# Optimization experiments

Measured on AMD Instinct MI355X. Metric: run time of the kernel, lower is better.

The kernel has to match this reference:

```python
import jax, jax.numpy as jnp
import numpy as np

B, E, H, KVH, S = 1, 4096, 32, 8, 2048
HD = E // H            # per-head dim = 128
KVE = KVH * HD         # kv projection embed dim = 1024


def setup_inputs() -> dict:
    key = jax.random.key(0)
    ks = jax.random.split(key, 10)
    std = 0.02
    return {
        "input_embeds": jax.random.normal(ks[0], (B, E, 1, S), jnp.float32),
        "cos": jax.random.uniform(ks[1], (HD, S), jnp.float32, -1.0, 1.0),
        "sin": jax.random.uniform(ks[2], (HD, S), jnp.float32, -1.0, 1.0),
        "wq": jax.random.normal(ks[3], (E, E), jnp.float32) * std,
        "bq": jnp.zeros((E,), jnp.float32),
        "wk": jax.random.normal(ks[4], (KVE, E), jnp.float32) * std,
        "wv": jax.random.normal(ks[5], (KVE, E), jnp.float32) * std,
        "bv": jnp.zeros((KVE,), jnp.float32),
        "wo": jax.random.normal(ks[6], (E, E), jnp.float32) * std,
        "bo": jnp.zeros((E,), jnp.float32),
    }


def _proj(w, x, b=None):
    # 1x1 Conv2d == channelwise linear on (B, C, 1, S)
    y = jnp.einsum('oc,bcxs->boxs', w, x)
    if b is not None:
        y = y + b[None, :, None, None]
    return y


def _rope(x, cos, sin):
    # x: (B, h, HD, S); rotate-half along head_dim axis
    half = x.shape[2] // 2
    x1, x2 = x[:, :, :half], x[:, :, half:]
    rot = jnp.concatenate([-x2, x1], axis=2)
    return x * cos[None, None] + rot * sin[None, None]


def reference(input_embeds, cos, sin, wq, bq, wk, wv, bv, wo, bo):
    b, e, _, s = input_embeds.shape
    hd = e // H
    q = _proj(wq, input_embeds, bq)          # (B, E, 1, S)
    k = _proj(wk, input_embeds)              # (B, KVE, 1, S)  (no bias)
    v = _proj(wv, input_embeds, bv)          # (B, KVE, 1, S)

    qh = q.reshape(b, H, hd, s)
    kh = k.reshape(b, KVH, hd, s)
    qh = _rope(qh, cos, sin)
    kh = _rope(kh, cos, sin)

    # GQA tiling: channel-block repeat => query head h uses kv head (h % KVH)
    rep = H // KVH
    kfull = jnp.tile(kh, (1, rep, 1, 1))                       # (B, H, HD, S)
    vfull = jnp.tile(v.reshape(b, KVH, hd, s), (1, rep, 1, 1))  # (B, H, HD, S)

    scale = 1.0 / np.sqrt(hd).astype(np.float32)
    scores = jnp.einsum('bhcq,bhck->bhqk', qh, kfull) * scale  # (B, H, S, S)
    causal = jnp.tril(jnp.ones((s, s), bool))
    scores = jnp.where(causal[None, None], scores, jnp.finfo(scores.dtype).min)
    w = jax.nn.softmax(scores, axis=-1)
    attn = jnp.einsum('bhqk,bhck->bhcq', w, vfull).reshape(b, e, 1, s)
    return _proj(wo, attn, bo)
```

## Files before the change

kernel.cpp:

```cpp
#include <hip/hip_runtime.h>


typedef unsigned short u16;
typedef unsigned int u32;
typedef __attribute__((ext_vector_type(8))) short bf16x8;
typedef __attribute__((ext_vector_type(4))) float f32x4;

__device__ __forceinline__ u16 f2b(float f){
  union { float f; u32 u; } v; v.f = f;
  u32 r = (v.u + 0x7FFFu + ((v.u >> 16) & 1u)) >> 16;
  return (u16)r;
}
__device__ __forceinline__ float b2f(u16 b){
  union { u32 u; float f; } v; v.u = ((u32)b) << 16;
  return v.f;
}

__device__ __forceinline__ void gld16(const void* g, void* l){
  __builtin_amdgcn_global_load_lds((const __attribute__((address_space(1))) u32*)g,
                                   (__attribute__((address_space(3))) u32*)l, 16, 0, 0);
}

__global__ __launch_bounds__(256) void cvt_w(const float* __restrict__ src,
                                             u16* __restrict__ dst, int n4)
{
  int i = blockIdx.x * 256 + threadIdx.x;
  if (i < n4){
    float4 v = *(const float4*)&src[(size_t)i * 4];
    ushort4 o; o.x = f2b(v.x); o.y = f2b(v.y); o.z = f2b(v.z); o.w = f2b(v.w);
    *(ushort4*)&dst[(size_t)i * 4] = o;
  }
}

__global__ __launch_bounds__(256) void transpose_x(const float* __restrict__ X,
                                                   u16* __restrict__ XT)
{
  __shared__ float lds[64][65];
  const int c0 = blockIdx.x * 64, s0 = blockIdx.y * 64;
  const int tid = threadIdx.x;
  {
    const int sg = tid & 15, cl = tid >> 4;
#pragma unroll
    for (int p = 0; p < 4; ++p){
      int c = cl + p * 16;
      float4 v = *(const float4*)&X[(size_t)(c0 + c) * 2048 + s0 + sg * 4];
      lds[sg*4+0][c] = v.x; lds[sg*4+1][c] = v.y;
      lds[sg*4+2][c] = v.z; lds[sg*4+3][c] = v.w;
    }
  }
  __syncthreads();
  {
    const int cg = tid & 15, sl = tid >> 4;
#pragma unroll
    for (int p = 0; p < 4; ++p){
      int s = sl + p * 16;
      ushort4 o;
      o.x = f2b(lds[s][cg*4+0]); o.y = f2b(lds[s][cg*4+1]);
      o.z = f2b(lds[s][cg*4+2]); o.w = f2b(lds[s][cg*4+3]);
      *(ushort4*)&XT[(size_t)(s0 + s) * 4096 + c0 + cg * 4] = o;
    }
  }
}

template<int EPI, int ABF>
__global__ __launch_bounds__(256) void gemm2(
    const u16* __restrict__ W0, const u16* __restrict__ W1, const u16* __restrict__ W2,
    const float* __restrict__ F0, const float* __restrict__ F1, const float* __restrict__ F2,
    const u16* __restrict__ B,
    const float* __restrict__ bias0, const float* __restrict__ bias2,
    u16* __restrict__ QTo, u16* __restrict__ KTo, u16* __restrict__ Vno,
    float* __restrict__ OUT)
{
  const int K = 4096;
  const int m0 = blockIdx.y * 128, n0 = blockIdx.x * 128;

  const u16* A16; const float* Af; int mA;
  if (EPI == 0){
    if (m0 < 4096)      { A16 = W0; Af = F0; mA = m0; }
    else if (m0 < 5120) { A16 = W1; Af = F1; mA = m0 - 4096; }
    else                { A16 = W2; Af = F2; mA = m0 - 5120; }
  } else { A16 = W0; Af = F0; mA = m0; }

  __shared__ __align__(16) u16 As[128 * 32];
  __shared__ __align__(16) u16 Bs[128 * 32];

  const int tid = threadIdx.x, lane = tid & 63, w = tid >> 6;
  const int wm = w >> 1, wn = w & 1, quad = lane >> 4, l15 = lane & 15;

  f32x4 acc[4][4];
#pragma unroll
  for (int mt = 0; mt < 4; ++mt)
#pragma unroll
    for (int nt = 0; nt < 4; ++nt)
      acc[mt][nt] = f32x4{0.f, 0.f, 0.f, 0.f};

  const int r0 = tid >> 2, gs0 = tid & 3;
  const int g0 = gs0 ^ ((r0 >> 1) & 3);
  const int r1 = r0 + 64;

  u16* ldsA0 = As + (size_t)(w * 64) * 8;
  u16* ldsA1 = As + (size_t)(w * 64 + 256) * 8;
  u16* ldsB0 = Bs + (size_t)(w * 64) * 8;
  u16* ldsB1 = Bs + (size_t)(w * 64 + 256) * 8;

  const u16* bsrc0 = &B[(size_t)(n0 + r0) * 4096 + g0 * 8];
  const u16* bsrc1 = &B[(size_t)(n0 + r1) * 4096 + g0 * 8];
  const u16* asrc0 = ABF ? &A16[(size_t)(mA + r0) * 4096 + g0 * 8] : nullptr;
  const u16* asrc1 = ABF ? &A16[(size_t)(mA + r1) * 4096 + g0 * 8] : nullptr;
  const float* afs0 = ABF ? nullptr : &Af[(size_t)(mA + r0) * 4096 + g0 * 8];
  const float* afs1 = ABF ? nullptr : &Af[(size_t)(mA + r1) * 4096 + g0 * 8];

  int aoff[4], boff[4];
#pragma unroll
  for (int mt = 0; mt < 4; ++mt){
    int row = wm * 64 + mt * 16 + l15;
    aoff[mt] = row * 32 + (quad ^ ((row >> 1) & 3)) * 8;
  }
#pragma unroll
  for (int nt = 0; nt < 4; ++nt){
    int row = wn * 64 + nt * 16 + l15;
    boff[nt] = row * 32 + (quad ^ ((row >> 1) & 3)) * 8;
  }

  for (int kt = 0; kt < K / 32; ++kt){
    const int k0 = kt * 32;
    if (ABF){
      gld16(asrc0 + k0, ldsA0);
      gld16(asrc1 + k0, ldsA1);
    } else {
      float4 v0 = *(const float4*)&afs0[k0];
      float4 v1 = *(const float4*)&afs0[k0 + 4];
      float4 v2 = *(const float4*)&afs1[k0];
      float4 v3 = *(const float4*)&afs1[k0 + 4];
      union { u16 u[8]; uint4 q; } p0, p1;
      p0.u[0]=f2b(v0.x); p0.u[1]=f2b(v0.y); p0.u[2]=f2b(v0.z); p0.u[3]=f2b(v0.w);
      p0.u[4]=f2b(v1.x); p0.u[5]=f2b(v1.y); p0.u[6]=f2b(v1.z); p0.u[7]=f2b(v1.w);
      p1.u[0]=f2b(v2.x); p1.u[1]=f2b(v2.y); p1.u[2]=f2b(v2.z); p1.u[3]=f2b(v2.w);
      p1.u[4]=f2b(v3.x); p1.u[5]=f2b(v3.y); p1.u[6]=f2b(v3.z); p1.u[7]=f2b(v3.w);
      *(uint4*)&As[(size_t)tid * 8] = p0.q;
      *(uint4*)&As[(size_t)(tid + 256) * 8] = p1.q;
    }
    gld16(bsrc0 + k0, ldsB0);
    gld16(bsrc1 + k0, ldsB1);
    __syncthreads();

    bf16x8 af[4], bfr[4];
#pragma unroll
    for (int mt = 0; mt < 4; ++mt) af[mt]  = *(const bf16x8*)&As[aoff[mt]];
#pragma unroll
    for (int nt = 0; nt < 4; ++nt) bfr[nt] = *(const bf16x8*)&Bs[boff[nt]];
#pragma unroll
    for (int mt = 0; mt < 4; ++mt)
#pragma unroll
      for (int nt = 0; nt < 4; ++nt)
        acc[mt][nt] = __builtin_amdgcn_mfma_f32_16x16x32_bf16(af[mt], bfr[nt], acc[mt][nt], 0, 0, 0);
    __syncthreads();
  }

  if (EPI == 0){
    if (m0 < 4096){
#pragma unroll
      for (int mt = 0; mt < 4; ++mt){
        int mb = m0 + wm * 64 + mt * 16 + quad * 4;
        float b0 = bias0[mb], b1 = bias0[mb+1], b2 = bias0[mb+2], b3 = bias0[mb+3];
#pragma unroll
        for (int nt = 0; nt < 4; ++nt){
          int n = n0 + wn * 64 + nt * 16 + l15;
          ushort4 o;
          o.x = f2b(acc[mt][nt][0] + b0); o.y = f2b(acc[mt][nt][1] + b1);
          o.z = f2b(acc[mt][nt][2] + b2); o.w = f2b(acc[mt][nt][3] + b3);
          *(ushort4*)&QTo[(size_t)n * 4096 + mb] = o;
        }
      }
    } else if (m0 < 5120){
#pragma unroll
      for (int mt = 0; mt < 4; ++mt){
        int mb = m0 - 4096 + wm * 64 + mt * 16 + quad * 4;
#pragma unroll
        for (int nt = 0; nt < 4; ++nt){
          int n = n0 + wn * 64 + nt * 16 + l15;
          ushort4 o;
          o.x = f2b(acc[mt][nt][0]); o.y = f2b(acc[mt][nt][1]);
          o.z = f2b(acc[mt][nt][2]); o.w = f2b(acc[mt][nt][3]);
          *(ushort4*)&KTo[(size_t)n * 1024 + mb] = o;
        }
      }
    } else {
#pragma unroll
      for (int mt = 0; mt < 4; ++mt)
#pragma unroll
        for (int r = 0; r < 4; ++r){
          int mv = m0 - 5120 + wm * 64 + mt * 16 + quad * 4 + r;
          float bb = bias2[mv];
#pragma unroll
          for (int nt = 0; nt < 4; ++nt){
            int n = n0 + wn * 64 + nt * 16 + l15;
            Vno[(size_t)mv * 2048 + n] = f2b(acc[mt][nt][r] + bb);
          }
        }
    }
  } else {
#pragma unroll
    for (int mt = 0; mt < 4; ++mt)
#pragma unroll
      for (int r = 0; r < 4; ++r){
        int m = m0 + wm * 64 + mt * 16 + quad * 4 + r;
        float bb = bias0[m];
#pragma unroll
        for (int nt = 0; nt < 4; ++nt){
          int n = n0 + wn * 64 + nt * 16 + l15;
          OUT[(size_t)m * 2048 + n] = acc[mt][nt][r] + bb;
        }
      }
  }
}

template<int EPI, int BM>
__global__ __launch_bounds__(512, 2) void gemm256(
    const u16* __restrict__ W0, const u16* __restrict__ W1, const u16* __restrict__ W2,
    const u16* __restrict__ Bmat,
    const float* __restrict__ bias0, const float* __restrict__ bias2,
    u16* __restrict__ QTo, u16* __restrict__ KTo, u16* __restrict__ Vno,
    float* __restrict__ OUT)
{
  const int NT = 64;
  const int m0 = blockIdx.y * BM, n0 = blockIdx.x * 256;
  constexpr int MT    = BM / 32;
  constexpr int ACH   = BM / 128;
  constexpr int SLICE = BM * 32;
  constexpr int ABUF  = 2 * SLICE;

  const u16* A16; int mA;
  if (EPI == 0){
    if (m0 < 4096)      { A16 = W0; mA = m0; }
    else if (m0 < 5120) { A16 = W1; mA = m0 - 4096; }
    else                { A16 = W2; mA = m0 - 5120; }
  } else { A16 = W0; mA = m0; }

  __shared__ __align__(16) u16 As[2 * ABUF];
  __shared__ __align__(16) u16 Bs[2 * 2 * 8192];

  const int tid = threadIdx.x, lane = tid & 63, w = tid >> 6;
  const int wm = w >> 2, wn = w & 3, quad = lane >> 4, l15 = lane & 15;

  f32x4 acc[MT][4];
#pragma unroll
  for (int mt = 0; mt < MT; ++mt)
#pragma unroll
    for (int nt = 0; nt < 4; ++nt)
      acc[mt][nt] = f32x4{0.f, 0.f, 0.f, 0.f};

  const int rowq = tid >> 2;
  const int kgA  = ((tid & 3) ^ ((rowq >> 1) & 3)) * 8;
  const u16* aG = &A16[(size_t)(mA + rowq) * 4096 + kgA];
  const u16* bG = &Bmat[(size_t)(n0 + rowq) * 4096 + kgA];
  u16* AsW = As + w * 512;
  u16* BsW = Bs + w * 512;

  int aoff[MT], boff[4];
#pragma unroll
  for (int mt = 0; mt < MT; ++mt){
    int row = wm * (BM / 2) + mt * 16 + l15;
    aoff[mt] = row * 32 + ((quad ^ ((row >> 1) & 3)) * 8);
  }
#pragma unroll
  for (int nt = 0; nt < 4; ++nt){
    int row = wn * 64 + nt * 16 + l15;
    boff[nt] = row * 32 + ((quad ^ ((row >> 1) & 3)) * 8);
  }

  auto stageT = [&](int b, int k0){
    u16* Ad = AsW + b * ABUF;
    u16* Bd = BsW + b * 16384;
    const u16* as_ = aG + k0;
    const u16* bs_ = bG + k0;
    gld16(as_, Ad);
    if constexpr (ACH == 2) gld16(as_ + 128 * 4096, Ad + 4096);
    gld16(bs_, Bd);
    gld16(bs_ + 128 * 4096, Bd + 4096);
    gld16(as_ + 32, Ad + SLICE);
    if constexpr (ACH == 2) gld16(as_ + 32 + 128 * 4096, Ad + SLICE + 4096);
    gld16(bs_ + 32, Bd + 8192);
    gld16(bs_ + 32 + 128 * 4096, Bd + 8192 + 4096);
  };

  stageT(0, 0);
  if constexpr (BM == 256) asm volatile("s_waitcnt vmcnt(4)" ::: "memory");
  else                     asm volatile("s_waitcnt vmcnt(3)" ::: "memory");
  __builtin_amdgcn_s_barrier();
  __builtin_amdgcn_sched_barrier(0);

#pragma unroll 1
  for (int t = 0; t < NT; ++t){
    const int buf = t & 1;
    const u16* Asl = As + buf * ABUF;
    const u16* Bsl = Bs + buf * 16384;

    {
      bf16x8 af[MT], bf[4];
#pragma unroll
      for (int mt = 0; mt < MT; ++mt) af[mt] = *(const bf16x8*)&Asl[aoff[mt]];
#pragma unroll
      for (int nt = 0; nt < 4; ++nt) bf[nt] = *(const bf16x8*)&Bsl[boff[nt]];
      if (t + 1 < NT) stageT((t + 1) & 1, (t + 1) * 64);
      __builtin_amdgcn_s_setprio(1);
#pragma unroll
      for (int mt = 0; mt < MT; ++mt)
#pragma unroll
        for (int nt = 0; nt < 4; ++nt)
          acc[mt][nt] = __builtin_amdgcn_mfma_f32_16x16x32_bf16(af[mt], bf[nt], acc[mt][nt], 0, 0, 0);
      __builtin_amdgcn_s_setprio(0);
      if (t + 1 < NT){
        if constexpr (BM == 256) asm volatile("s_waitcnt vmcnt(8)" ::: "memory");
        else                     asm volatile("s_waitcnt vmcnt(6)" ::: "memory");
      } else {
        asm volatile("s_waitcnt vmcnt(0)" ::: "memory");
      }
      __builtin_amdgcn_s_barrier();
      __builtin_amdgcn_sched_barrier(0);
    }
    {
      bf16x8 af[MT], bf[4];
#pragma unroll
      for (int mt = 0; mt < MT; ++mt) af[mt] = *(const bf16x8*)&Asl[SLICE + aoff[mt]];
#pragma unroll
      for (int nt = 0; nt < 4; ++nt) bf[nt] = *(const bf16x8*)&Bsl[8192 + boff[nt]];
      __builtin_amdgcn_s_setprio(1);
#pragma unroll
      for (int mt = 0; mt < MT; ++mt)
#pragma unroll
        for (int nt = 0; nt < 4; ++nt)
          acc[mt][nt] = __builtin_amdgcn_mfma_f32_16x16x32_bf16(af[mt], bf[nt], acc[mt][nt], 0, 0, 0);
      __builtin_amdgcn_s_setprio(0);
      if (t + 1 < NT){
        if constexpr (BM == 256) asm volatile("s_waitcnt vmcnt(4)" ::: "memory");
        else                     asm volatile("s_waitcnt vmcnt(3)" ::: "memory");
      }
      __builtin_amdgcn_s_barrier();
      __builtin_amdgcn_sched_barrier(0);
    }
  }

  if (EPI == 0){
    if (m0 < 4096){
#pragma unroll
      for (int mt = 0; mt < MT; ++mt){
        int mb = m0 + wm * (BM / 2) + mt * 16 + quad * 4;
        float b0 = bias0[mb], b1 = bias0[mb+1], b2 = bias0[mb+2], b3 = bias0[mb+3];
#pragma unroll
        for (int nt = 0; nt < 4; ++nt){
          int n = n0 + wn * 64 + nt * 16 + l15;
          ushort4 o;
          o.x = f2b(acc[mt][nt][0] + b0); o.y = f2b(acc[mt][nt][1] + b1);
          o.z = f2b(acc[mt][nt][2] + b2); o.w = f2b(acc[mt][nt][3] + b3);
          *(ushort4*)&QTo[(size_t)n * 4096 + mb] = o;
        }
      }
    } else if (m0 < 5120){
#pragma unroll
      for (int mt = 0; mt < MT; ++mt){
        int mb = m0 - 4096 + wm * (BM / 2) + mt * 16 + quad * 4;
#pragma unroll
        for (int nt = 0; nt < 4; ++nt){
          int n = n0 + wn * 64 + nt * 16 + l15;
          ushort4 o;
          o.x = f2b(acc[mt][nt][0]); o.y = f2b(acc[mt][nt][1]);
          o.z = f2b(acc[mt][nt][2]); o.w = f2b(acc[mt][nt][3]);
          *(ushort4*)&KTo[(size_t)n * 1024 + mb] = o;
        }
      }
    } else {
#pragma unroll
      for (int mt = 0; mt < MT; ++mt)
#pragma unroll
        for (int r = 0; r < 4; ++r){
          int mv = m0 - 5120 + wm * (BM / 2) + mt * 16 + quad * 4 + r;
          float bb = bias2[mv];
#pragma unroll
          for (int nt = 0; nt < 4; ++nt){
            int n = n0 + wn * 64 + nt * 16 + l15;
            Vno[(size_t)mv * 2048 + n] = f2b(acc[mt][nt][r] + bb);
          }
        }
    }
  } else {
#pragma unroll
    for (int mt = 0; mt < MT; ++mt)
#pragma unroll
      for (int r = 0; r < 4; ++r){
        int m = m0 + wm * (BM / 2) + mt * 16 + quad * 4 + r;
        float bb = bias0[m];
#pragma unroll
        for (int nt = 0; nt < 4; ++nt){
          int n = n0 + wn * 64 + nt * 16 + l15;
          OUT[(size_t)m * 2048 + n] = acc[mt][nt][r] + bb;
        }
      }
  }
}

__global__ __launch_bounds__(256) void rope_kernel(u16* __restrict__ QT,
                                                   u16* __restrict__ KT,
                                                   const float* __restrict__ cosp,
                                                   const float* __restrict__ sinp)
{
  const float qscale = 0.08838834764831845f * 1.4426950408889634f;
  int gid = blockIdx.x * 256 + threadIdx.x;
  const int NQ = 2048 * 32 * 64;
  if (gid < NQ){
    int c = gid & 63, hh = (gid >> 6) & 31, s = gid >> 11;
    size_t base = (size_t)s * 4096 + hh * 128 + c;
    float x1 = b2f(QT[base]), x2 = b2f(QT[base + 64]);
    float c1 = cosp[c * 2048 + s],        s1 = sinp[c * 2048 + s];
    float c2 = cosp[(c + 64) * 2048 + s], s2 = sinp[(c + 64) * 2048 + s];
    QT[base]      = f2b((x1 * c1 - x2 * s1) * qscale);
    QT[base + 64] = f2b((x2 * c2 + x1 * s2) * qscale);
  } else {
    int g = gid - NQ;
    int c = g & 63, hh = (g >> 6) & 7, s = g >> 9;
    size_t base = (size_t)s * 1024 + hh * 128 + c;
    float x1 = b2f(KT[base]), x2 = b2f(KT[base + 64]);
    float c1 = cosp[c * 2048 + s],        s1 = sinp[c * 2048 + s];
    float c2 = cosp[(c + 64) * 2048 + s], s2 = sinp[(c + 64) * 2048 + s];
    KT[base]      = f2b(x1 * c1 - x2 * s1);
    KT[base + 64] = f2b(x2 * c2 + x1 * s2);
  }
}

__global__ __launch_bounds__(512, 2) void attn5(const u16* __restrict__ QT,
                                                const u16* __restrict__ KT,
                                                const u16* __restrict__ Vn,
                                                u16* __restrict__ AT)
{
  const int h = blockIdx.x;
  const int g = blockIdx.y;
  const int kvh = h & 7;
  const int tid = threadIdx.x;
  const int w = tid >> 6, lane = tid & 63;
  const int quad = lane >> 4, l15 = lane & 15;

  const int t = 8 * g + w;
  const int e = t >> 1;
  const int i0 = t * 32;
  const int U = 4 * g + 4;

  __shared__ __align__(16) u16 Ks[2][64 * 128];
  __shared__ __align__(16) u16 Vs[128 * 64];
  __shared__ __align__(16) u16 Ps[8][16][64];

  bf16x8 qa[2][4];
#pragma unroll
  for (int mt = 0; mt < 2; ++mt)
#pragma unroll
    for (int kc = 0; kc < 4; ++kc)
      qa[mt][kc] = *(const bf16x8*)&QT[(size_t)(i0 + mt * 16 + l15) * 4096
                                       + h * 128 + kc * 32 + quad * 8];

  f32x4 o[2][9];
#pragma unroll
  for (int mt = 0; mt < 2; ++mt)
#pragma unroll
    for (int ct = 0; ct < 9; ++ct)
      o[mt][ct] = f32x4{0.f, 0.f, 0.f, 0.f};

  bf16x8 ones;
#pragma unroll
  for (int z = 0; z < 8; ++z) ones[z] = (short)0x3F80;

  const int krl = lane >> 4, kgl = lane & 15;
  const int vrl = lane >> 3, vgl = lane & 7;

  auto stageK = [&](int buf, int j0){
#pragma unroll
    for (int qq = 0; qq < 2; ++qq){
      int r = w * 8 + qq * 4 + krl;
      gld16(&KT[(size_t)(j0 + r) * 1024 + kvh * 128 + ((kgl ^ (r & 7)) * 8)],
            &Ks[buf][(size_t)(w * 8 + qq * 4) * 128]);
    }
  };
  auto stageV = [&](int j0){
#pragma unroll
    for (int qq = 0; qq < 2; ++qq){
      int r = w * 16 + qq * 8 + vrl;
      gld16(&Vn[(size_t)(kvh * 128 + r) * 2048 + j0 + ((vgl ^ (r & 7)) * 8)],
            &Vs[(size_t)(w * 16 + qq * 8) * 64]);
    }
  };

  stageK(0, 0);
  for (int u = 0; u < U; ++u){
    __syncthreads();
    stageV(u * 64);
    if (u + 1 < U) stageK((u + 1) & 1, (u + 1) * 64);

    const int j0 = u * 64;
    const bool act = (u <= e);
    const u16* Kb = &Ks[u & 1][0];

    f32x4 s[2][4];
    bf16x8 pa[2][2];
    if (act){
#pragma unroll
      for (int mt = 0; mt < 2; ++mt)
#pragma unroll
        for (int nt = 0; nt < 4; ++nt)
          s[mt][nt] = f32x4{0.f, 0.f, 0.f, 0.f};
#pragma unroll
      for (int nt = 0; nt < 4; ++nt){
        bf16x8 kb[4];
#pragma unroll
        for (int kc = 0; kc < 4; ++kc){
          int row = nt * 16 + l15;
          kb[kc] = *(const bf16x8*)&Kb[row * 128 + (((kc * 4 + quad) ^ (row & 7)) * 8)];
        }
        __builtin_amdgcn_s_setprio(1);
#pragma unroll
        for (int kc = 0; kc < 4; ++kc){
          s[0][nt] = __builtin_amdgcn_mfma_f32_16x16x32_bf16(qa[0][kc], kb[kc], s[0][nt], 0, 0, 0);
          s[1][nt] = __builtin_amdgcn_mfma_f32_16x16x32_bf16(qa[1][kc], kb[kc], s[1][nt], 0, 0, 0);
        }
        __builtin_amdgcn_s_setprio(0);
      }
      const bool maskit = (u == e);
#pragma unroll
      for (int mt = 0; mt < 2; ++mt){
#pragma unroll
        for (int nt = 0; nt < 4; ++nt)
#pragma unroll
          for (int r = 0; r < 4; ++r){
            float pv = exp2f(fminf(s[mt][nt][r], 60.0f));
            if (maskit && (j0 + nt * 16 + l15 > i0 + mt * 16 + quad * 4 + r)) pv = 0.0f;
            int col = nt * 16 + l15, rowp = quad * 4 + r;
            Ps[w][rowp][((col >> 3) ^ (rowp & 7)) * 8 + (col & 7)] = f2b(pv);
          }
#pragma unroll
        for (int kc = 0; kc < 2; ++kc){
          pa[mt][kc] = *(const bf16x8*)&Ps[w][l15][((kc * 4 + quad) ^ (l15 & 7)) * 8];
          o[mt][8] = __builtin_amdgcn_mfma_f32_16x16x32_bf16(pa[mt][kc], ones, o[mt][8], 0, 0, 0);
        }
      }
    }
    if (u + 1 < U) asm volatile("s_waitcnt vmcnt(2)" ::: "memory");
    else           asm volatile("s_waitcnt vmcnt(0)" ::: "memory");
    __builtin_amdgcn_s_barrier();
    __builtin_amdgcn_sched_barrier(0);

    if (act){
#pragma unroll
      for (int ct = 0; ct < 8; ++ct){
#pragma unroll
        for (int kc = 0; kc < 2; ++kc){
          int row = ct * 16 + l15;
          bf16x8 vb = *(const bf16x8*)&Vs[row * 64 + (((kc * 4 + quad) ^ (row & 7)) * 8)];
          __builtin_amdgcn_s_setprio(1);
          o[0][ct] = __builtin_amdgcn_mfma_f32_16x16x32_bf16(pa[0][kc], vb, o[0][ct], 0, 0, 0);
          o[1][ct] = __builtin_amdgcn_mfma_f32_16x16x32_bf16(pa[1][kc], vb, o[1][ct], 0, 0, 0);
          __builtin_amdgcn_s_setprio(0);
        }
      }
      if (u == e){
#pragma unroll
        for (int mt = 0; mt < 2; ++mt){
          float rinv[4];
#pragma unroll
          for (int r = 0; r < 4; ++r) rinv[r] = 1.0f / o[mt][8][r];
#pragma unroll
          for (int ct = 0; ct < 8; ++ct)
#pragma unroll
            for (int r = 0; r < 4; ++r){
              int i = i0 + mt * 16 + quad * 4 + r;
              AT[(size_t)i * 4096 + h * 128 + ct * 16 + l15] = f2b(o[mt][ct][r] * rinv[r]);
            }
        }
      }
    }
  }
}

extern "C" void kernel_launch(void* const* d_in, const int* in_sizes, int n_in,
                              void* d_out, int out_size, void* d_ws, size_t ws_size,
                              hipStream_t stream)
{
  const float* X    = (const float*)d_in[0];
  const float* cosp = (const float*)d_in[1];
  const float* sinp = (const float*)d_in[2];
  const float* wq   = (const float*)d_in[3];
  const float* bq   = (const float*)d_in[4];
  const float* wk   = (const float*)d_in[5];
  const float* wv   = (const float*)d_in[6];
  const float* bv   = (const float*)d_in[7];
  const float* wo   = (const float*)d_in[8];
  const float* bo   = (const float*)d_in[9];
  float* out = (float*)d_out;

  char* ws = (char*)d_ws;
  const size_t MB = 1u << 20;

  if (ws_size >= 88 * MB){
    u16* W16Q = (u16*)(ws);
    u16* W16K = (u16*)(ws + 32 * MB);
    u16* W16V = (u16*)(ws + 40 * MB);
    u16* XT   = (u16*)(ws + 48 * MB);
    u16* QT   = (u16*)(ws + 64 * MB);
    u16* KT   = (u16*)(ws + 80 * MB);
    u16* Vn   = (u16*)(ws + 84 * MB);
    u16* AT   = (u16*)(ws + 48 * MB);
    u16* WO16 = (u16*)(ws);

    cvt_w<<<16384, 256, 0, stream>>>(wq, W16Q, 4194304);
    cvt_w<<< 4096, 256, 0, stream>>>(wk, W16K, 1048576);
    cvt_w<<< 4096, 256, 0, stream>>>(wv, W16V, 1048576);
    transpose_x<<<dim3(64, 32), 256, 0, stream>>>(X, XT);
    gemm256<0, 256><<<dim3(8, 24), 512, 0, stream>>>(W16Q, W16K, W16V, XT,
                                                     bq, bv, QT, KT, Vn, nullptr);
    cvt_w<<<16384, 256, 0, stream>>>(wo, WO16, 4194304);
    rope_kernel<<<20480, 256, 0, stream>>>(QT, KT, cosp, sinp);
    attn5<<<dim3(32, 8), 512, 0, stream>>>(QT, KT, Vn, AT);
    gemm256<1, 128><<<dim3(8, 32), 512, 0, stream>>>(WO16, nullptr, nullptr, AT,
                                                     bo, nullptr, nullptr, nullptr, nullptr, out);
  } else {
    u16* XT = (u16*)(ws);
    u16* QT = (u16*)(ws + 16 * MB);
    u16* KT = (u16*)(ws + 32 * MB);
    u16* Vn = (u16*)(ws + 36 * MB);
    u16* AT = (u16*)(ws + 40 * MB);

    transpose_x<<<dim3(64, 32), 256, 0, stream>>>(X, XT);
    gemm2<0,0><<<dim3(16, 48), 256, 0, stream>>>(nullptr, nullptr, nullptr, wq, wk, wv,
                                                 XT, bq, bv, QT, KT, Vn, nullptr);
    rope_kernel<<<20480, 256, 0, stream>>>(QT, KT, cosp, sinp);
    attn5<<<dim3(32, 8), 512, 0, stream>>>(QT, KT, Vn, AT);
    gemm2<1,0><<<dim3(16, 32), 256, 0, stream>>>(nullptr, nullptr, nullptr, wo, nullptr, nullptr,
                                                 AT, bo, nullptr, nullptr, nullptr, nullptr, out);
  }
}
```

Measured before the change: 598.5 us.

## Split GEMM K-step into four quarter phases interleaving LDS reads, global prefetch, MFMA

Restructures the gemm256 main loop from two half-step phases into four phases. Each phase loads a subset of A/B fragments from LDS, issues a slice of the next tile's global-to-LDS loads, then runs a smaller group of MFMAs. The aim is to spread memory issue across the compute and keep the waves in step through barriers, cutting fragment register pressure and stalls. The cost is twice as many barriers per K-step and a more fragile vmcnt/lgkmcnt accounting.

```diff
diff --git a/kernel.cpp b/kernel.cpp
--- a/kernel.cpp
+++ b/kernel.cpp
@@ -226,7 +226,6 @@
   const int NT = 64;
   const int m0 = blockIdx.y * BM, n0 = blockIdx.x * 256;
   constexpr int MT    = BM / 32;
-  constexpr int ACH   = BM / 128;
   constexpr int SLICE = BM * 32;
   constexpr int ABUF  = 2 * SLICE;
 
@@ -269,24 +268,23 @@
     boff[nt] = row * 32 + ((quad ^ ((row >> 1) & 3)) * 8);
   }
 
-  auto stageT = [&](int b, int k0){
-    u16* Ad = AsW + b * ABUF;
-    u16* Bd = BsW + b * 16384;
-    const u16* as_ = aG + k0;
-    const u16* bs_ = bG + k0;
-    gld16(as_, Ad);
-    if constexpr (ACH == 2) gld16(as_ + 128 * 4096, Ad + 4096);
-    gld16(bs_, Bd);
-    gld16(bs_ + 128 * 4096, Bd + 4096);
-    gld16(as_ + 32, Ad + SLICE);
-    if constexpr (ACH == 2) gld16(as_ + 32 + 128 * 4096, Ad + SLICE + 4096);
-    gld16(bs_ + 32, Bd + 8192);
-    gld16(bs_ + 32 + 128 * 4096, Bd + 8192 + 4096);
-  };
-
-  stageT(0, 0);
-  if constexpr (BM == 256) asm volatile("s_waitcnt vmcnt(4)" ::: "memory");
-  else                     asm volatile("s_waitcnt vmcnt(3)" ::: "memory");
+  {
+    u16* Ad = AsW; u16* Bd = BsW;
+    if constexpr (BM == 256){
+      gld16(aG, Ad); gld16(aG + 128 * 4096, Ad + 4096);
+      gld16(bG, Bd); gld16(bG + 128 * 4096, Bd + 4096);
+      gld16(aG + 32, Ad + SLICE); gld16(aG + 32 + 128 * 4096, Ad + SLICE + 4096);
+      gld16(bG + 32, Bd + 8192);  gld16(bG + 32 + 128 * 4096, Bd + 8192 + 4096);
+      asm volatile("s_waitcnt vmcnt(4)" ::: "memory");
+    } else {
+      gld16(aG, Ad); gld16(bG, Bd);
+      gld16(bG + 128 * 4096, Bd + 4096);
+      gld16(aG + 32, Ad + SLICE);
+      gld16(bG + 32, Bd + 8192);
+      gld16(bG + 32 + 128 * 4096, Bd + 8192 + 4096);
+      asm volatile("s_waitcnt vmcnt(3)" ::: "memory");
+    }
+  }
   __builtin_amdgcn_s_barrier();
   __builtin_amdgcn_sched_barrier(0);
 
@@ -295,50 +293,150 @@
     const int buf = t & 1;
     const u16* Asl = As + buf * ABUF;
     const u16* Bsl = Bs + buf * 16384;
-
-    {
-      bf16x8 af[MT], bf[4];
-#pragma unroll
-      for (int mt = 0; mt < MT; ++mt) af[mt] = *(const bf16x8*)&Asl[aoff[mt]];
-#pragma unroll
-      for (int nt = 0; nt < 4; ++nt) bf[nt] = *(const bf16x8*)&Bsl[boff[nt]];
-      if (t + 1 < NT) stageT((t + 1) & 1, (t + 1) * 64);
-      __builtin_amdgcn_s_setprio(1);
-#pragma unroll
-      for (int mt = 0; mt < MT; ++mt)
+    const int nb = buf ^ 1;
+    const bool more = (t + 1 < NT);
+    u16* Ad = AsW + nb * ABUF;
+    u16* Bd = BsW + nb * 16384;
+    const u16* as_ = aG + (t + 1) * 64;
+    const u16* bs_ = bG + (t + 1) * 64;
+
+    bf16x8 af[4], bf[4];
+
+#pragma unroll
+    for (int i = 0; i < 4; ++i) af[i] = *(const bf16x8*)&Asl[aoff[i]];
+    if constexpr (BM == 256){
+#pragma unroll
+      for (int i = 0; i < 4; ++i) bf[i] = *(const bf16x8*)&Bsl[boff[i]];
+      if (more){ gld16(as_, Ad); gld16(as_ + 128 * 4096, Ad + 4096); }
+    } else {
+      bf[0] = *(const bf16x8*)&Bsl[boff[0]];
+      bf[1] = *(const bf16x8*)&Bsl[boff[1]];
+      if (more){ gld16(as_, Ad); gld16(bs_, Bd); }
+    }
+    __builtin_amdgcn_s_barrier();
+    asm volatile("s_waitcnt lgkmcnt(0)" ::: "memory");
+    __builtin_amdgcn_sched_barrier(0);
+    __builtin_amdgcn_s_setprio(1);
+    if constexpr (BM == 256){
+#pragma unroll
+      for (int mt = 0; mt < 4; ++mt)
 #pragma unroll
         for (int nt = 0; nt < 4; ++nt)
           acc[mt][nt] = __builtin_amdgcn_mfma_f32_16x16x32_bf16(af[mt], bf[nt], acc[mt][nt], 0, 0, 0);
-      __builtin_amdgcn_s_setprio(0);
-      if (t + 1 < NT){
-        if constexpr (BM == 256) asm volatile("s_waitcnt vmcnt(8)" ::: "memory");
-        else                     asm volatile("s_waitcnt vmcnt(6)" ::: "memory");
-      } else {
-        asm volatile("s_waitcnt vmcnt(0)" ::: "memory");
-      }
-      __builtin_amdgcn_s_barrier();
-      __builtin_amdgcn_sched_barrier(0);
-    }
-    {
-      bf16x8 af[MT], bf[4];
-#pragma unroll
-      for (int mt = 0; mt < MT; ++mt) af[mt] = *(const bf16x8*)&Asl[SLICE + aoff[mt]];
-#pragma unroll
-      for (int nt = 0; nt < 4; ++nt) bf[nt] = *(const bf16x8*)&Bsl[8192 + boff[nt]];
-      __builtin_amdgcn_s_setprio(1);
-#pragma unroll
-      for (int mt = 0; mt < MT; ++mt)
+    } else {
+#pragma unroll
+      for (int mt = 0; mt < 4; ++mt)
+#pragma unroll
+        for (int nt = 0; nt < 2; ++nt)
+          acc[mt][nt] = __builtin_amdgcn_mfma_f32_16x16x32_bf16(af[mt], bf[nt], acc[mt][nt], 0, 0, 0);
+    }
+    __builtin_amdgcn_s_setprio(0);
+    __builtin_amdgcn_s_barrier();
+    __builtin_amdgcn_sched_barrier(0);
+
+    if constexpr (BM == 256){
+#pragma unroll
+      for (int i = 0; i < 4; ++i) af[i] = *(const bf16x8*)&Asl[aoff[4 + i]];
+      if (more){ gld16(bs_, Bd); gld16(bs_ + 128 * 4096, Bd + 4096); }
+    } else {
+      bf[2] = *(const bf16x8*)&Bsl[boff[2]];
+      bf[3] = *(const bf16x8*)&Bsl[boff[3]];
+      if (more){ gld16(bs_ + 128 * 4096, Bd + 4096); }
+    }
+    __builtin_amdgcn_s_barrier();
+    asm volatile("s_waitcnt lgkmcnt(0)" ::: "memory");
+    __builtin_amdgcn_sched_barrier(0);
+    __builtin_amdgcn_s_setprio(1);
+    if constexpr (BM == 256){
+#pragma unroll
+      for (int mt = 0; mt < 4; ++mt)
+#pragma unroll
+        for (int nt = 0; nt < 4; ++nt)
+          acc[4 + mt][nt] = __builtin_amdgcn_mfma_f32_16x16x32_bf16(af[mt], bf[nt], acc[4 + mt][nt], 0, 0, 0);
+    } else {
+#pragma unroll
+      for (int mt = 0; mt < 4; ++mt)
+#pragma unroll
+        for (int nt = 2; nt < 4; ++nt)
+          acc[mt][nt] = __builtin_amdgcn_mfma_f32_16x16x32_bf16(af[mt], bf[nt], acc[mt][nt], 0, 0, 0);
+    }
+    __builtin_amdgcn_s_setprio(0);
+    if (more){
+      if constexpr (BM == 256) asm volatile("s_waitcnt vmcnt(4)" ::: "memory");
+      else                     asm volatile("s_waitcnt vmcnt(3)" ::: "memory");
+    } else {
+      asm volatile("s_waitcnt vmcnt(0)" ::: "memory");
+    }
+    __builtin_amdgcn_s_barrier();
+    __builtin_amdgcn_sched_barrier(0);
+
+#pragma unroll
+    for (int i = 0; i < 4; ++i) af[i] = *(const bf16x8*)&Asl[SLICE + aoff[i]];
+    if constexpr (BM == 256){
+#pragma unroll
+      for (int i = 0; i < 4; ++i) bf[i] = *(const bf16x8*)&Bsl[8192 + boff[i]];
+      if (more){ gld16(as_ + 32, Ad + SLICE); gld16(as_ + 32 + 128 * 4096, Ad + SLICE + 4096); }
+    } else {
+      bf[0] = *(const bf16x8*)&Bsl[8192 + boff[0]];
+      bf[1] = *(const bf16x8*)&Bsl[8192 + boff[1]];
+      if (more){ gld16(as_ + 32, Ad + SLICE); gld16(bs_ + 32, Bd + 8192); }
+    }
+    __builtin_amdgcn_s_barrier();
+    asm volatile("s_waitcnt lgkmcnt(0)" ::: "memory");
+    __builtin_amdgcn_sched_barrier(0);
+    __builtin_amdgcn_s_setprio(1);
+    if constexpr (BM == 256){
+#pragma unroll
+      for (int mt = 0; mt < 4; ++mt)
 #pragma unroll
         for (int nt = 0; nt < 4; ++nt)
           acc[mt][nt] = __builtin_amdgcn_mfma_f32_16x16x32_bf16(af[mt], bf[nt], acc[mt][nt], 0, 0, 0);
-      __builtin_amdgcn_s_setprio(0);
-      if (t + 1 < NT){
-        if constexpr (BM == 256) asm volatile("s_waitcnt vmcnt(4)" ::: "memory");
-        else                     asm volatile("s_waitcnt vmcnt(3)" ::: "memory");
-      }
-      __builtin_amdgcn_s_barrier();
-      __builtin_amdgcn_sched_barrier(0);
-    }
+    } else {
+#pragma unroll
+      for (int mt = 0; mt < 4; ++mt)
+#pragma unroll
+        for (int nt = 0; nt < 2; ++nt)
+          acc[mt][nt] = __builtin_amdgcn_mfma_f32_16x16x32_bf16(af[mt], bf[nt], acc[mt][nt], 0, 0, 0);
+    }
+    __builtin_amdgcn_s_setprio(0);
+    __builtin_amdgcn_s_barrier();
+    __builtin_amdgcn_sched_barrier(0);
+
+    if constexpr (BM == 256){
+#pragma unroll
+      for (int i = 0; i < 4; ++i) af[i] = *(const bf16x8*)&Asl[SLICE + aoff[4 + i]];
+      if (more){ gld16(bs_ + 32, Bd + 8192); gld16(bs_ + 32 + 128 * 4096, Bd + 8192 + 4096); }
+    } else {
+      bf[2] = *(const bf16x8*)&Bsl[8192 + boff[2]];
+      bf[3] = *(const bf16x8*)&Bsl[8192 + boff[3]];
+      if (more){ gld16(bs_ + 32 + 128 * 4096, Bd + 8192 + 4096); }
+    }
+    __builtin_amdgcn_s_barrier();
+    asm volatile("s_waitcnt lgkmcnt(0)" ::: "memory");
+    __builtin_amdgcn_sched_barrier(0);
+    __builtin_amdgcn_s_setprio(1);
+    if constexpr (BM == 256){
+#pragma unroll
+      for (int mt = 0; mt < 4; ++mt)
+#pragma unroll
+        for (int nt = 0; nt < 4; ++nt)
+          acc[4 + mt][nt] = __builtin_amdgcn_mfma_f32_16x16x32_bf16(af[mt], bf[nt], acc[4 + mt][nt], 0, 0, 0);
+    } else {
+#pragma unroll
+      for (int mt = 0; mt < 4; ++mt)
+#pragma unroll
+        for (int nt = 2; nt < 4; ++nt)
+          acc[mt][nt] = __builtin_amdgcn_mfma_f32_16x16x32_bf16(af[mt], bf[nt], acc[mt][nt], 0, 0, 0);
+    }
+    __builtin_amdgcn_s_setprio(0);
+    if (more){
+      if constexpr (BM == 256) asm volatile("s_waitcnt vmcnt(4)" ::: "memory");
+      else                     asm volatile("s_waitcnt vmcnt(3)" ::: "memory");
+    } else {
+      asm volatile("s_waitcnt vmcnt(0)" ::: "memory");
+    }
+    __builtin_amdgcn_s_barrier();
+    __builtin_amdgcn_sched_barrier(0);
   }
 
   if (EPI == 0){
```

After: 592.1 us. No clear change (-1.1%).
